# Optimization experiments

Hardware: AMD Instinct MI355X
Metric: run time of the kernel (lower is better)

## Reference

```python
import jax, jax.numpy as jnp
import numpy as np

NEG = -1e20

def _rope(x):
    # x: (N, L, H, D). Original buffers use inv_freq over D with D/2 entries;
    # sin/cos tiled to full D to broadcast (original code's einsum was under-specified for 4D).
    L, D = x.shape[1], x.shape[3]
    inv_freq = 1.0 / (10000.0 ** (jnp.arange(0, D, 2, dtype=jnp.float32) / D))
    t = jnp.arange(L, dtype=jnp.float32)
    freqs = t[:, None] * inv_freq[None, :]            # (L, D/2)
    sin = jnp.concatenate([jnp.sin(freqs)] * 2, -1)[None, :, None, :]  # (1,L,1,D)
    cos = jnp.concatenate([jnp.cos(freqs)] * 2, -1)[None, :, None, :]
    return x * cos + jnp.flip(x, -1) * sin

def setup_inputs() -> dict:
    key = jax.random.key(0)
    ks = jax.random.split(key, 8)
    N, L, E, H = 2, 1024, 2048, 16
    D = E // H
    s = 0.02
    return {
        "values": jax.random.normal(ks[0], (N, L, E), jnp.float32),
        "keys": jax.random.normal(ks[1], (N, L, E), jnp.float32),
        "queries": jax.random.normal(ks[2], (N, L, E), jnp.float32),
        "mask": jax.random.randint(ks[3], (N, 1, L, L), 0, 2, jnp.int32),
        "Wv": jax.random.normal(ks[4], (D, D), jnp.float32) * s,
        "Wk": jax.random.normal(ks[5], (D, D), jnp.float32) * s,
        "Wq": jax.random.normal(ks[6], (D, D), jnp.float32) * s,
        "Wo": jax.random.normal(ks[7], (E, E), jnp.float32) * s,
        "bo": jnp.zeros((E,), jnp.float32),
    }

def reference(values, keys, queries, mask, Wv, Wk, Wq, Wo, bo):
    N, L, E = queries.shape
    H = 16
    D = E // H
    v = values.reshape(N, L, H, D)
    k = keys.reshape(N, L, H, D)
    q = queries.reshape(N, L, H, D)
    q = _rope(q)
    k = _rope(k)
    # per-head linears (nn.Linear: x @ W.T)
    v = jnp.einsum('nlhd,od->nlho', v, Wv)
    k = jnp.einsum('nlhd,od->nlho', k, Wk)
    q = jnp.einsum('nlhd,od->nlho', q, Wq)
    energy = jnp.einsum('nqhd,nkhd->nhqk', q, k)
    energy = jnp.where(mask == 0, NEG, energy)
    attn = jax.nn.softmax(energy / jnp.sqrt(jnp.float32(E)), axis=3)
    out = jnp.einsum('nhqk,nkhd->nqhd', attn, v).reshape(N, L, E)
    return out @ Wo.T + bo
```

## Files before the change

### kernel.cpp

```cpp
#include <hip/hip_runtime.h>

#define LQ 1024
#define EMB 2048
#define NH 16
#define HD 128
#define RSCALE 0.022097086912079608f

typedef unsigned short u16x8 __attribute__((ext_vector_type(8)));
typedef __bf16 bf16x8 __attribute__((ext_vector_type(8)));
typedef float f32x4 __attribute__((ext_vector_type(4)));
typedef short s16x4 __attribute__((ext_vector_type(4)));

typedef const __attribute__((address_space(1))) unsigned int* gas_t;
typedef __attribute__((address_space(3))) unsigned int* las_t;

__device__ __forceinline__ void glds16(const void* g, void* l){
  __builtin_amdgcn_global_load_lds((gas_t)g, (las_t)l, 16, 0, 0);
}
__device__ __forceinline__ unsigned short f2b(float f){
  unsigned int x = __float_as_uint(f);
  return (unsigned short)((x + 0x7fffu + ((x >> 16) & 1u)) >> 16);
}
__device__ __forceinline__ unsigned short f2bu(float f){
  union { __bf16 h; unsigned short u; } c; c.h = (__bf16)f; return c.u;
}
__device__ __forceinline__ short f2bs(float f){
  union { __bf16 h; short s; } c; c.h = (__bf16)f; return c.s;
}
__device__ __forceinline__ bf16x8 as_bf(u16x8 u){
  union { u16x8 u; bf16x8 b; } c; c.u = u; return c.b;
}
__device__ __forceinline__ f32x4 mfma16(s16x4 a, s16x4 b, f32x4 c){
  return __builtin_amdgcn_mfma_f32_16x16x16bf16_1k(a, b, c, 0, 0, 0);
}

__global__ __launch_bounds__(256) void k_proj(
    const float* __restrict__ vals, const float* __restrict__ keys,
    const float* __restrict__ qrys,
    const float* __restrict__ Wv, const float* __restrict__ Wk,
    const float* __restrict__ Wq,
    const float* __restrict__ Wo, const int* __restrict__ M,
    unsigned short* __restrict__ kp, unsigned short* __restrict__ qp,
    unsigned short* __restrict__ vtF, unsigned short* __restrict__ Wob,
    unsigned long long* __restrict__ Mb)
{
  __shared__ unsigned short Xs[64 * 136];
  __shared__ unsigned short Ws[128 * 136];
  __shared__ float scC[4 * 128], scS[4 * 128];
  int t = threadIdx.x;
  int which = blockIdx.y;

  if (which == 3) {
    int bx = blockIdx.x;
    #pragma unroll
    for (int k = 0; k < 8; ++k) {
      int i = (bx * 2048 + k * 256 + t) * 4;
      float4 f = *(const float4*)&Wo[i];
      ushort4 u;
      u.x = f2bu(f.x); u.y = f2bu(f.y); u.z = f2bu(f.z); u.w = f2bu(f.w);
      *(ushort4*)&Wob[i] = u;
    }
    int w = t >> 6, lane = t & 63;
    #pragma unroll
    for (int i = 0; i < 16; ++i) {
      int w_idx = bx * 64 + w * 16 + i;
      int n = w_idx >> 14, row = (w_idx >> 4) & 1023, wc = w_idx & 15;
      int v = M[(size_t)n * (LQ * LQ) + (size_t)row * LQ + wc * 64 + lane];
      unsigned long long b = __ballot(v != 0);
      if (lane == 0) Mb[w_idx] = b;
    }
    return;
  }

  const float* X; const float* W; bool rope;
  if (which == 0)      { X = vals; W = Wv; rope = false; }
  else if (which == 1) { X = keys; W = Wk; rope = true;  }
  else                 { X = qrys; W = Wq; rope = true;  }
  float qs = (which == 2) ? RSCALE : 1.0f;

  int w = t >> 6, lane = t & 63, quad = lane >> 4, n16 = lane & 15;

  #pragma unroll
  for (int i = 0; i < 8; ++i) {
    int ci = t + 256 * i;
    int row = ci >> 4, ch = ci & 15;
    float4 a = *(const float4*)&W[row * 128 + ch * 8];
    float4 b = *(const float4*)&W[row * 128 + ch * 8 + 4];
    u16x8 u;
    u[0]=f2bu(a.x); u[1]=f2bu(a.y); u[2]=f2bu(a.z); u[3]=f2bu(a.w);
    u[4]=f2bu(b.x); u[5]=f2bu(b.y); u[6]=f2bu(b.z); u[7]=f2bu(b.w);
    *(u16x8*)&Ws[row * 136 + ch * 8] = u;
  }
  if (rope) {
    int l0 = (blockIdx.x * 4) & 1023;
    #pragma unroll
    for (int i = 0; i < 2; ++i) {
      int idx = t + 256 * i;
      int li = idx >> 7, d = idx & 127, j = d & 63;
      float inv = 1.0f / powf(10000.0f, (float)(2 * j) * 0.0078125f);
      float ang = (float)(l0 + li) * inv;
      scC[idx] = cosf(ang);
      scS[idx] = sinf(ang);
    }
  }
  __syncthreads();

  if (which == 0) {
    int bh = blockIdx.x >> 4, kt = blockIdx.x & 15;
    int n = bh >> 4, h = bh & 15;
    #pragma unroll
    for (int i = 0; i < 8; ++i) {
      int fi = t + 256 * i;
      int row = fi >> 5, dq = (fi & 31) * 4;
      size_t gr = (size_t)n * 16384 + (size_t)(kt * 64 + row) * 16 + h;
      float4 x = *(const float4*)&X[gr * HD + dq];
      ushort4 u;
      u.x = f2bu(x.x); u.y = f2bu(x.y); u.z = f2bu(x.z); u.w = f2bu(x.w);
      *(ushort4*)&Xs[row * 136 + dq] = u;
    }
  } else {
    int m0 = blockIdx.x * 64;
    #pragma unroll
    for (int i = 0; i < 8; ++i) {
      int fi = t + 256 * i;
      int row = fi >> 5, dq = (fi & 31) * 4;
      int gr = m0 + row;
      float4 x = *(const float4*)&X[(size_t)gr * HD + dq];
      int li = row >> 4;
      float4 xm = *(const float4*)&X[(size_t)gr * HD + (124 - dq)];
      float4 c  = *(const float4*)&scC[li * 128 + dq];
      float4 s  = *(const float4*)&scS[li * 128 + dq];
      ushort4 u;
      u.x = f2bu(x.x * c.x + xm.w * s.x);
      u.y = f2bu(x.y * c.y + xm.z * s.y);
      u.z = f2bu(x.z * c.z + xm.y * s.z);
      u.w = f2bu(x.w * c.w + xm.x * s.w);
      *(ushort4*)&Xs[row * 136 + dq] = u;
    }
  }
  __syncthreads();

  f32x4 of[4][2];
  #pragma unroll
  for (int a = 0; a < 4; ++a)
    { of[a][0] = (f32x4){0.f,0.f,0.f,0.f}; of[a][1] = (f32x4){0.f,0.f,0.f,0.f}; }

  #pragma unroll
  for (int kd = 0; kd < 4; ++kd) {
    bf16x8 bfr[2];
    #pragma unroll
    for (int b2 = 0; b2 < 2; ++b2)
      bfr[b2] = as_bf(*(const u16x8*)&Ws[(w * 32 + b2 * 16 + n16) * 136 + kd * 32 + quad * 8]);
    #pragma unroll
    for (int a = 0; a < 4; ++a) {
      bf16x8 af = as_bf(*(const u16x8*)&Xs[(a * 16 + n16) * 136 + kd * 32 + quad * 8]);
      of[a][0] = __builtin_amdgcn_mfma_f32_16x16x32_bf16(af, bfr[0], of[a][0], 0, 0, 0);
      of[a][1] = __builtin_amdgcn_mfma_f32_16x16x32_bf16(af, bfr[1], of[a][1], 0, 0, 0);
    }
  }

  if (which == 0) {
    int bh = blockIdx.x >> 4, kt = blockIdx.x & 15;
    size_t vbase = (size_t)bh * (LQ * HD) + (size_t)kt * 8192;
    #pragma unroll
    for (int a = 0; a < 4; ++a) {
      u16x8 u;
      u[0]=f2bu(of[a][0][0]); u[1]=f2bu(of[a][0][1]);
      u[2]=f2bu(of[a][0][2]); u[3]=f2bu(of[a][0][3]);
      u[4]=f2bu(of[a][1][0]); u[5]=f2bu(of[a][1][1]);
      u[6]=f2bu(of[a][1][2]); u[7]=f2bu(of[a][1][3]);
      *(u16x8*)&vtF[vbase + (size_t)(((a * 4 + w) * 64 + (quad * 16 + n16)) * 8)] = u;
    }
  } else {
    unsigned short* OUT = (which == 1) ? kp : qp;
    int m0 = blockIdx.x * 64;
    __syncthreads();
    #pragma unroll
    for (int a = 0; a < 4; ++a)
      #pragma unroll
      for (int b2 = 0; b2 < 2; ++b2)
        #pragma unroll
        for (int r = 0; r < 4; ++r)
          Ws[(a * 16 + quad * 4 + r) * 136 + w * 32 + b2 * 16 + n16] =
              f2bu(of[a][b2][r] * qs);
    __syncthreads();
    #pragma unroll
    for (int i = 0; i < 4; ++i) {
      int chunk = t + 256 * i;
      int row = chunk >> 4, dc = chunk & 15;
      u16x8 v = *(const u16x8*)&Ws[row * 136 + dc * 8];
      int m = m0 + row;
      int n = m >> 14, l = (m >> 4) & 1023, h = m & 15;
      *(u16x8*)&OUT[(((size_t)(n * NH + h)) * LQ + l) * HD + dc * 8] = v;
    }
  }
}

__global__ __launch_bounds__(512) void k_attn(
    const unsigned short* __restrict__ qp, const unsigned short* __restrict__ kp,
    const unsigned short* __restrict__ vtF, const unsigned long long* __restrict__ Mb,
    unsigned short* __restrict__ ao)
{
  __shared__ unsigned short KsF[2][8192];
  __shared__ unsigned short VsF[2][8192];
  __shared__ float ls[8][16];
  int t = threadIdx.x, w = t >> 6, lane = t & 63, quad = lane >> 4, n16 = lane & 15;
  int grp = w >> 2, wq = w & 3;
  int lin = blockIdx.y * gridDim.x + blockIdx.x;
  int xcd = lin & 7, j = lin >> 3;
  int bh = xcd + 8 * (j >> 4);
  int q0 = (j & 15) * 64;
  int nIdx = bh >> 4, h = bh & 15;
  size_t base = (size_t)bh * LQ * HD;
  const unsigned short* Q = qp + base;
  const unsigned short* K = kp + base;
  const unsigned short* VF = vtF + base;

  bf16x8 qf[4];
  #pragma unroll
  for (int kd = 0; kd < 4; ++kd)
    qf[kd] = as_bf(*(const u16x8*)&Q[(size_t)(q0 + wq * 16 + n16) * HD + kd * 32 + quad * 8]);

  const unsigned long long* MbRow =
      Mb + ((size_t)nIdx * LQ + q0 + wq * 16 + n16) * 16;

  f32x4 of[8];
  #pragma unroll
  for (int c = 0; c < 8; ++c) of[c] = (f32x4){0.f, 0.f, 0.f, 0.f};
  float lp = 0.f;

  for (int p = 0; p < 8; ++p) {
    int k0 = p * 128;
    __syncthreads();
    #pragma unroll
    for (int jj = 0; jj < 2; ++jj) {
      int kt = 2 * p + jj;
      #pragma unroll
      for (int i = 0; i < 2; ++i) {
        int D = t + 512 * i;
        int nn = D & 15, qq = (D >> 4) & 3, cc = (D >> 6) & 3, kd = D >> 8;
        glds16(&K[(size_t)(k0 + jj * 64 + cc * 16 + nn) * HD + (kd * 4 + qq) * 8],
               &KsF[jj][(size_t)D * 8]);
        glds16(&VF[(size_t)kt * 8192 + (size_t)D * 8],
               &VsF[jj][(size_t)D * 8]);
      }
    }
    unsigned long long mq = MbRow[2 * p + grp];
    __syncthreads();

    unsigned long long msh = mq >> (quad * 4);

    f32x4 sf[4];
    #pragma unroll
    for (int c = 0; c < 4; ++c) sf[c] = (f32x4){0.f, 0.f, 0.f, 0.f};
    __builtin_amdgcn_s_setprio(1);
    #pragma unroll
    for (int kd = 0; kd < 4; ++kd) {
      #pragma unroll
      for (int c = 0; c < 4; ++c) {
        bf16x8 kv = as_bf(*(const u16x8*)&KsF[grp][((kd * 4 + c) * 64 + lane) * 8]);
        sf[c] = __builtin_amdgcn_mfma_f32_16x16x32_bf16(kv, qf[kd], sf[c], 0, 0, 0);
      }
    }
    __builtin_amdgcn_s_setprio(0);
    #pragma unroll
    for (int c = 0; c < 4; ++c) {
      s16x4 pa;
      #pragma unroll
      for (int r = 0; r < 4; ++r) {
        int bit = (int)((msh >> (c * 16 + r)) & 1ull);
        float p = bit ? __expf(sf[c][r]) : 0.f;
        lp += p;
        pa[r] = f2bs(p);
      }
      __builtin_amdgcn_s_setprio(1);
      #pragma unroll
      for (int c2p = 0; c2p < 4; ++c2p) {
        u16x8 vv2 = *(const u16x8*)&VsF[grp][((c * 4 + c2p) * 64 + lane) * 8];
        s16x4 vlo = { (short)vv2[0], (short)vv2[1], (short)vv2[2], (short)vv2[3] };
        s16x4 vhi = { (short)vv2[4], (short)vv2[5], (short)vv2[6], (short)vv2[7] };
        of[2 * c2p]     = mfma16(pa, vlo, of[2 * c2p]);
        of[2 * c2p + 1] = mfma16(pa, vhi, of[2 * c2p + 1]);
      }
      __builtin_amdgcn_s_setprio(0);
    }
  }

  __syncthreads();
  {
    float s = lp;
    s += __shfl_xor(s, 16);
    s += __shfl_xor(s, 32);
    ls[w][n16] = s;
  }
  float* OF = (float*)&KsF[0][0];
  if (grp == 1) {
    #pragma unroll
    for (int c2 = 0; c2 < 8; ++c2) {
      #pragma unroll
      for (int r = 0; r < 4; ++r) {
        OF[(wq * 16 + quad * 4 + r) * 128 + c2 * 16 + n16] = of[c2][r];
      }
    }
  }
  __syncthreads();
  if (grp == 0) {
    float linv[4];
    #pragma unroll
    for (int r = 0; r < 4; ++r)
      linv[r] = 1.0f / fmaxf(ls[wq][quad * 4 + r] + ls[wq + 4][quad * 4 + r], 1e-30f);
    #pragma unroll
    for (int c2 = 0; c2 < 8; ++c2) {
      #pragma unroll
      for (int r = 0; r < 4; ++r) {
        float v = of[c2][r] + OF[(wq * 16 + quad * 4 + r) * 128 + c2 * 16 + n16];
        ao[((size_t)(nIdx * LQ + q0 + wq * 16 + quad * 4 + r)) * EMB + h * HD + c2 * 16 + n16] =
            f2b(v * linv[r]);
      }
    }
  }
}

__global__ __launch_bounds__(256) void k_outproj(
    const unsigned short* __restrict__ ao, const unsigned short* __restrict__ Wob,
    const float* __restrict__ bo, float* __restrict__ out)
{
  __shared__ unsigned short As[2][128 * 64];
  __shared__ unsigned short Bs[2][64 * 64];
  int t = threadIdx.x;
  int w = t >> 6, lane = t & 63, quad = lane >> 4, n16 = lane & 15;
  int wm = w >> 1, wo = w & 1;
  int m0 = blockIdx.x * 128, o0 = blockIdx.y * 64;
  int ub = (t & 192);

  f32x4 of[4][2];
  #pragma unroll
  for (int a = 0; a < 4; ++a)
    { of[a][0] = (f32x4){0.f,0.f,0.f,0.f}; of[a][1] = (f32x4){0.f,0.f,0.f,0.f}; }

  #pragma unroll
  for (int i = 0; i < 4; ++i) {
    int ci = t + 256 * i;
    int row = ci >> 3, ch = (ci & 7) ^ (row & 7);
    glds16(&ao[(size_t)(m0 + row) * EMB + ch * 8], &As[0][(ub + 256 * i) * 8]);
  }
  #pragma unroll
  for (int i = 0; i < 2; ++i) {
    int ci = t + 256 * i;
    int row = ci >> 3, ch = (ci & 7) ^ (row & 7);
    glds16(&Wob[(size_t)(o0 + row) * EMB + ch * 8], &Bs[0][(ub + 256 * i) * 8]);
  }

  for (int kt = 0; kt < 32; ++kt) {
    int cur = kt & 1;
    __syncthreads();
    if (kt < 31) {
      int k1 = (kt + 1) * 64;
      #pragma unroll
      for (int i = 0; i < 4; ++i) {
        int ci = t + 256 * i;
        int row = ci >> 3, ch = (ci & 7) ^ (row & 7);
        glds16(&ao[(size_t)(m0 + row) * EMB + k1 + ch * 8], &As[1 - cur][(ub + 256 * i) * 8]);
      }
      #pragma unroll
      for (int i = 0; i < 2; ++i) {
        int ci = t + 256 * i;
        int row = ci >> 3, ch = (ci & 7) ^ (row & 7);
        glds16(&Wob[(size_t)(o0 + row) * EMB + k1 + ch * 8], &Bs[1 - cur][(ub + 256 * i) * 8]);
      }
    }
    #pragma unroll
    for (int kd = 0; kd < 2; ++kd) {
      int slot0 = (kd * 4 + quad);
      bf16x8 af[4], bf[2];
      #pragma unroll
      for (int a = 0; a < 4; ++a)
        af[a] = as_bf(*(const u16x8*)&As[cur][(wm * 64 + a * 16 + n16) * 64 + (slot0 ^ (n16 & 7)) * 8]);
      #pragma unroll
      for (int b = 0; b < 2; ++b)
        bf[b] = as_bf(*(const u16x8*)&Bs[cur][(wo * 32 + b * 16 + n16) * 64 + (slot0 ^ (n16 & 7)) * 8]);
      #pragma unroll
      for (int a = 0; a < 4; ++a)
        #pragma unroll
        for (int b = 0; b < 2; ++b)
          of[a][b] = __builtin_amdgcn_mfma_f32_16x16x32_bf16(af[a], bf[b], of[a][b], 0, 0, 0);
    }
  }

  float bb[2] = { bo[o0 + wo * 32 + n16], bo[o0 + wo * 32 + 16 + n16] };
  #pragma unroll
  for (int a = 0; a < 4; ++a) {
    #pragma unroll
    for (int b = 0; b < 2; ++b) {
      #pragma unroll
      for (int r = 0; r < 4; ++r) {
        out[(size_t)(m0 + wm * 64 + a * 16 + quad * 4 + r) * EMB
            + o0 + wo * 32 + b * 16 + n16] = of[a][b][r] + bb[b];
      }
    }
  }
}

extern "C" void kernel_launch(void* const* d_in, const int* in_sizes, int n_in,
                              void* d_out, int out_size, void* d_ws, size_t ws_size,
                              hipStream_t stream) {
  (void)in_sizes; (void)n_in; (void)out_size; (void)ws_size;
  const float* vals = (const float*)d_in[0];
  const float* keys = (const float*)d_in[1];
  const float* qrys = (const float*)d_in[2];
  const int*   mask = (const int*)d_in[3];
  const float* Wv   = (const float*)d_in[4];
  const float* Wk   = (const float*)d_in[5];
  const float* Wq   = (const float*)d_in[6];
  const float* Wo   = (const float*)d_in[7];
  const float* bo   = (const float*)d_in[8];
  float* out = (float*)d_out;

  unsigned short* U  = (unsigned short*)d_ws;
  unsigned short* qp = U;
  unsigned short* kp = U + 4194304;
  unsigned short* vtF= U + 12582912;
  unsigned short* ao = U + 16777216;
  unsigned short* Wob= U + 20971520;
  unsigned long long* Mb = (unsigned long long*)(U + 25165824);

  k_proj    <<<dim3(512, 4), dim3(256), 0, stream>>>(vals, keys, qrys, Wv, Wk, Wq,
                                                     Wo, mask, kp, qp, vtF, Wob, Mb);
  k_attn    <<<dim3(16, 32), dim3(512), 0, stream>>>(qp, kp, vtF, Mb, ao);
  k_outproj <<<dim3(16, 32), dim3(256), 0, stream>>>(ao, Wob, bo, out);
}
```

Before: 194.8 us.

## Process four tiles per projection block and stage attention output through LDS

The projection kernel now handles four 64-row tiles per block, so the grid shrinks by a factor of four. This amortizes the per-block weight conversion to bf16 and the RoPE sin/cos table setup. The mask ballot loop is batched so eight loads are in flight before the ballots. The attention epilogue now writes normalized bf16 output into shared memory first, then issues coalesced 16-byte global stores instead of scattered 2-byte ones. The tradeoff is fewer blocks (less parallelism, possible tail effects) and more shared memory for the larger sin/cos tables.

```diff
diff --git a/kernel.cpp b/kernel.cpp
--- a/kernel.cpp
+++ b/kernel.cpp
@@ -46,28 +46,34 @@
 {
   __shared__ unsigned short Xs[64 * 136];
   __shared__ unsigned short Ws[128 * 136];
-  __shared__ float scC[4 * 128], scS[4 * 128];
+  __shared__ float scC[16 * 128], scS[16 * 128];
   int t = threadIdx.x;
   int which = blockIdx.y;
 
   if (which == 3) {
     int bx = blockIdx.x;
-    #pragma unroll
-    for (int k = 0; k < 8; ++k) {
-      int i = (bx * 2048 + k * 256 + t) * 4;
+    #pragma unroll 4
+    for (int k = 0; k < 32; ++k) {
+      int i = (bx * 8192 + k * 256 + t) * 4;
       float4 f = *(const float4*)&Wo[i];
       ushort4 u;
       u.x = f2bu(f.x); u.y = f2bu(f.y); u.z = f2bu(f.z); u.w = f2bu(f.w);
       *(ushort4*)&Wob[i] = u;
     }
     int w = t >> 6, lane = t & 63;
-    #pragma unroll
-    for (int i = 0; i < 16; ++i) {
-      int w_idx = bx * 64 + w * 16 + i;
-      int n = w_idx >> 14, row = (w_idx >> 4) & 1023, wc = w_idx & 15;
-      int v = M[(size_t)n * (LQ * LQ) + (size_t)row * LQ + wc * 64 + lane];
-      unsigned long long b = __ballot(v != 0);
-      if (lane == 0) Mb[w_idx] = b;
+    for (int i0 = 0; i0 < 64; i0 += 8) {
+      int v[8];
+      #pragma unroll
+      for (int j = 0; j < 8; ++j) {
+        int w_idx = bx * 256 + w * 64 + i0 + j;
+        int n = w_idx >> 14, row = (w_idx >> 4) & 1023, wc = w_idx & 15;
+        v[j] = M[(size_t)n * (LQ * LQ) + (size_t)row * LQ + wc * 64 + lane];
+      }
+      #pragma unroll
+      for (int j = 0; j < 8; ++j) {
+        unsigned long long b = __ballot(v[j] != 0);
+        if (lane == 0) Mb[bx * 256 + w * 64 + i0 + j] = b;
+      }
     }
     return;
   }
@@ -92,9 +98,9 @@
     *(u16x8*)&Ws[row * 136 + ch * 8] = u;
   }
   if (rope) {
-    int l0 = (blockIdx.x * 4) & 1023;
-    #pragma unroll
-    for (int i = 0; i < 2; ++i) {
+    int l0 = (blockIdx.x * 16) & 1023;
+    #pragma unroll
+    for (int i = 0; i < 8; ++i) {
       int idx = t + 256 * i;
       int li = idx >> 7, d = idx & 127, j = d & 63;
       float inv = 1.0f / powf(10000.0f, (float)(2 * j) * 0.0078125f);
@@ -105,93 +111,98 @@
   }
   __syncthreads();
 
-  if (which == 0) {
-    int bh = blockIdx.x >> 4, kt = blockIdx.x & 15;
-    int n = bh >> 4, h = bh & 15;
-    #pragma unroll
-    for (int i = 0; i < 8; ++i) {
-      int fi = t + 256 * i;
-      int row = fi >> 5, dq = (fi & 31) * 4;
-      size_t gr = (size_t)n * 16384 + (size_t)(kt * 64 + row) * 16 + h;
-      float4 x = *(const float4*)&X[gr * HD + dq];
-      ushort4 u;
-      u.x = f2bu(x.x); u.y = f2bu(x.y); u.z = f2bu(x.z); u.w = f2bu(x.w);
-      *(ushort4*)&Xs[row * 136 + dq] = u;
-    }
-  } else {
-    int m0 = blockIdx.x * 64;
-    #pragma unroll
-    for (int i = 0; i < 8; ++i) {
-      int fi = t + 256 * i;
-      int row = fi >> 5, dq = (fi & 31) * 4;
-      int gr = m0 + row;
-      float4 x = *(const float4*)&X[(size_t)gr * HD + dq];
-      int li = row >> 4;
-      float4 xm = *(const float4*)&X[(size_t)gr * HD + (124 - dq)];
-      float4 c  = *(const float4*)&scC[li * 128 + dq];
-      float4 s  = *(const float4*)&scS[li * 128 + dq];
-      ushort4 u;
-      u.x = f2bu(x.x * c.x + xm.w * s.x);
-      u.y = f2bu(x.y * c.y + xm.z * s.y);
-      u.z = f2bu(x.z * c.z + xm.y * s.z);
-      u.w = f2bu(x.w * c.w + xm.x * s.w);
-      *(ushort4*)&Xs[row * 136 + dq] = u;
-    }
-  }
-  __syncthreads();
-
-  f32x4 of[4][2];
-  #pragma unroll
-  for (int a = 0; a < 4; ++a)
-    { of[a][0] = (f32x4){0.f,0.f,0.f,0.f}; of[a][1] = (f32x4){0.f,0.f,0.f,0.f}; }
-
-  #pragma unroll
-  for (int kd = 0; kd < 4; ++kd) {
-    bf16x8 bfr[2];
-    #pragma unroll
-    for (int b2 = 0; b2 < 2; ++b2)
-      bfr[b2] = as_bf(*(const u16x8*)&Ws[(w * 32 + b2 * 16 + n16) * 136 + kd * 32 + quad * 8]);
-    #pragma unroll
-    for (int a = 0; a < 4; ++a) {
-      bf16x8 af = as_bf(*(const u16x8*)&Xs[(a * 16 + n16) * 136 + kd * 32 + quad * 8]);
-      of[a][0] = __builtin_amdgcn_mfma_f32_16x16x32_bf16(af, bfr[0], of[a][0], 0, 0, 0);
-      of[a][1] = __builtin_amdgcn_mfma_f32_16x16x32_bf16(af, bfr[1], of[a][1], 0, 0, 0);
-    }
-  }
-
-  if (which == 0) {
-    int bh = blockIdx.x >> 4, kt = blockIdx.x & 15;
-    size_t vbase = (size_t)bh * (LQ * HD) + (size_t)kt * 8192;
-    #pragma unroll
-    for (int a = 0; a < 4; ++a) {
-      u16x8 u;
-      u[0]=f2bu(of[a][0][0]); u[1]=f2bu(of[a][0][1]);
-      u[2]=f2bu(of[a][0][2]); u[3]=f2bu(of[a][0][3]);
-      u[4]=f2bu(of[a][1][0]); u[5]=f2bu(of[a][1][1]);
-      u[6]=f2bu(of[a][1][2]); u[7]=f2bu(of[a][1][3]);
-      *(u16x8*)&vtF[vbase + (size_t)(((a * 4 + w) * 64 + (quad * 16 + n16)) * 8)] = u;
-    }
-  } else {
-    unsigned short* OUT = (which == 1) ? kp : qp;
-    int m0 = blockIdx.x * 64;
+  int bh0 = blockIdx.x >> 2;
+  for (int tile = 0; tile < 4; ++tile) {
+    int bx4 = blockIdx.x * 4 + tile;
+    int m0 = bx4 * 64;
+    int kt0 = bx4 & 15;
+
+    if (which == 0) {
+      int n = bh0 >> 4, h = bh0 & 15;
+      #pragma unroll
+      for (int i = 0; i < 8; ++i) {
+        int fi = t + 256 * i;
+        int row = fi >> 5, dq = (fi & 31) * 4;
+        size_t gr = (size_t)n * 16384 + (size_t)(kt0 * 64 + row) * 16 + h;
+        float4 x = *(const float4*)&X[gr * HD + dq];
+        ushort4 u;
+        u.x = f2bu(x.x); u.y = f2bu(x.y); u.z = f2bu(x.z); u.w = f2bu(x.w);
+        *(ushort4*)&Xs[row * 136 + dq] = u;
+      }
+    } else {
+      #pragma unroll
+      for (int i = 0; i < 8; ++i) {
+        int fi = t + 256 * i;
+        int row = fi >> 5, dq = (fi & 31) * 4;
+        int gr = m0 + row;
+        float4 x = *(const float4*)&X[(size_t)gr * HD + dq];
+        int li = tile * 4 + (row >> 4);
+        float4 xm = *(const float4*)&X[(size_t)gr * HD + (124 - dq)];
+        float4 c  = *(const float4*)&scC[li * 128 + dq];
+        float4 s  = *(const float4*)&scS[li * 128 + dq];
+        ushort4 u;
+        u.x = f2bu(x.x * c.x + xm.w * s.x);
+        u.y = f2bu(x.y * c.y + xm.z * s.y);
+        u.z = f2bu(x.z * c.z + xm.y * s.z);
+        u.w = f2bu(x.w * c.w + xm.x * s.w);
+        *(ushort4*)&Xs[row * 136 + dq] = u;
+      }
+    }
     __syncthreads();
+
+    f32x4 of[4][2];
     #pragma unroll
     for (int a = 0; a < 4; ++a)
+      { of[a][0] = (f32x4){0.f,0.f,0.f,0.f}; of[a][1] = (f32x4){0.f,0.f,0.f,0.f}; }
+
+    #pragma unroll
+    for (int kd = 0; kd < 4; ++kd) {
+      bf16x8 bfr[2];
       #pragma unroll
       for (int b2 = 0; b2 < 2; ++b2)
+        bfr[b2] = as_bf(*(const u16x8*)&Ws[(w * 32 + b2 * 16 + n16) * 136 + kd * 32 + quad * 8]);
+      #pragma unroll
+      for (int a = 0; a < 4; ++a) {
+        bf16x8 af = as_bf(*(const u16x8*)&Xs[(a * 16 + n16) * 136 + kd * 32 + quad * 8]);
+        of[a][0] = __builtin_amdgcn_mfma_f32_16x16x32_bf16(af, bfr[0], of[a][0], 0, 0, 0);
+        of[a][1] = __builtin_amdgcn_mfma_f32_16x16x32_bf16(af, bfr[1], of[a][1], 0, 0, 0);
+      }
+    }
+
+    if (which == 0) {
+      size_t vbase = (size_t)bh0 * (LQ * HD) + (size_t)kt0 * 8192;
+      #pragma unroll
+      for (int a = 0; a < 4; ++a) {
+        u16x8 u;
+        u[0]=f2bu(of[a][0][0]); u[1]=f2bu(of[a][0][1]);
+        u[2]=f2bu(of[a][0][2]); u[3]=f2bu(of[a][0][3]);
+        u[4]=f2bu(of[a][1][0]); u[5]=f2bu(of[a][1][1]);
+        u[6]=f2bu(of[a][1][2]); u[7]=f2bu(of[a][1][3]);
+        *(u16x8*)&vtF[vbase + (size_t)(((a * 4 + w) * 64 + (quad * 16 + n16)) * 8)] = u;
+      }
+      __syncthreads();
+    } else {
+      unsigned short* OUT = (which == 1) ? kp : qp;
+      __syncthreads();
+      #pragma unroll
+      for (int a = 0; a < 4; ++a)
         #pragma unroll
-        for (int r = 0; r < 4; ++r)
-          Ws[(a * 16 + quad * 4 + r) * 136 + w * 32 + b2 * 16 + n16] =
-              f2bu(of[a][b2][r] * qs);
-    __syncthreads();
-    #pragma unroll
-    for (int i = 0; i < 4; ++i) {
-      int chunk = t + 256 * i;
-      int row = chunk >> 4, dc = chunk & 15;
-      u16x8 v = *(const u16x8*)&Ws[row * 136 + dc * 8];
-      int m = m0 + row;
-      int n = m >> 14, l = (m >> 4) & 1023, h = m & 15;
-      *(u16x8*)&OUT[(((size_t)(n * NH + h)) * LQ + l) * HD + dc * 8] = v;
+        for (int b2 = 0; b2 < 2; ++b2)
+          #pragma unroll
+          for (int r = 0; r < 4; ++r)
+            Xs[(a * 16 + quad * 4 + r) * 136 + w * 32 + b2 * 16 + n16] =
+                f2bu(of[a][b2][r] * qs);
+      __syncthreads();
+      #pragma unroll
+      for (int i = 0; i < 4; ++i) {
+        int chunk = t + 256 * i;
+        int row = chunk >> 4, dc = chunk & 15;
+        u16x8 v = *(const u16x8*)&Xs[row * 136 + dc * 8];
+        int m = m0 + row;
+        int n = m >> 14, l = (m >> 4) & 1023, h = m & 15;
+        *(u16x8*)&OUT[(((size_t)(n * NH + h)) * LQ + l) * HD + dc * 8] = v;
+      }
+      __syncthreads();
     }
   }
 }
@@ -294,6 +305,7 @@
     ls[w][n16] = s;
   }
   float* OF = (float*)&KsF[0][0];
+  unsigned short* AO = &VsF[0][0];
   if (grp == 1) {
     #pragma unroll
     for (int c2 = 0; c2 < 8; ++c2) {
@@ -314,10 +326,17 @@
       #pragma unroll
       for (int r = 0; r < 4; ++r) {
         float v = of[c2][r] + OF[(wq * 16 + quad * 4 + r) * 128 + c2 * 16 + n16];
-        ao[((size_t)(nIdx * LQ + q0 + wq * 16 + quad * 4 + r)) * EMB + h * HD + c2 * 16 + n16] =
-            f2b(v * linv[r]);
-      }
-    }
+        AO[(wq * 16 + quad * 4 + r) * 128 + c2 * 16 + n16] = f2bu(v * linv[r]);
+      }
+    }
+  }
+  __syncthreads();
+  #pragma unroll
+  for (int i = 0; i < 2; ++i) {
+    int chunk = t + 512 * i;
+    int q = chunk >> 4, dc = chunk & 15;
+    u16x8 v = *(const u16x8*)&AO[q * 128 + dc * 8];
+    *(u16x8*)&ao[((size_t)(nIdx * LQ + q0 + q)) * EMB + h * HD + dc * 8] = v;
   }
 }
 
@@ -424,7 +443,7 @@
   unsigned short* Wob= U + 20971520;
   unsigned long long* Mb = (unsigned long long*)(U + 25165824);
 
-  k_proj    <<<dim3(512, 4), dim3(256), 0, stream>>>(vals, keys, qrys, Wv, Wk, Wq,
+  k_proj    <<<dim3(128, 4), dim3(256), 0, stream>>>(vals, keys, qrys, Wv, Wk, Wq,
                                                      Wo, mask, kp, qp, vtF, Wob, Mb);
   k_attn    <<<dim3(16, 32), dim3(512), 0, stream>>>(qp, kp, vtF, Mb, ao);
   k_outproj <<<dim3(16, 32), dim3(256), 0, stream>>>(ao, Wob, bo, out);
```

Measured after the change: 188.1 us, median of 2. 3.4% less time.
